# Kernel tuning notes

Measured on AMD Instinct MI355X. Metric: run time of the kernel, lower is better.

Reference implementation:

```python
import jax, jax.numpy as jnp
import numpy as np

N_EMBD = 2048
HEAD_SIZE = 64  # ln1.weight.shape[0] // n_head = 2048 // 32


def setup_inputs() -> dict:
    key = jax.random.key(0)
    ks = jax.random.split(key, 10)
    B, S, D = 4, 2048, N_EMBD
    return {
        'x': jax.random.normal(ks[0], (B, S, D), jnp.float32),
        'state': jax.random.normal(ks[1], (B, 2 + HEAD_SIZE, D), jnp.float32),
        'time_maa_x': jax.random.uniform(ks[2], (D,), jnp.float32),
        'time_maa_w1': jax.random.normal(ks[3], (D, 160), jnp.float32) * 0.02,
        'time_maa_w2': jax.random.normal(ks[4], (5, 32, D), jnp.float32) * 0.02,
        'maa_k': jax.random.uniform(ks[5], (D,), jnp.float32),
        'maa_w': jax.random.uniform(ks[6], (D,), jnp.float32),
        'maa_v': jax.random.uniform(ks[7], (D,), jnp.float32),
        'maa_r': jax.random.uniform(ks[8], (D,), jnp.float32),
        'maa_g': jax.random.uniform(ks[9], (D,), jnp.float32),
        'i': 0,
    }


def reference(x, state, time_maa_x, time_maa_w1, time_maa_w2,
              maa_k, maa_w, maa_v, maa_r, maa_g, i):
    B, S, D = x.shape
    i1 = (2 + HEAD_SIZE) * i + 1  # state row holding last token of this layer
    # token shift: sx[t] = x[t-1] - x[t], with state row for t=0
    sx = jnp.concatenate([(state[:, i1] - x[:, 0])[:, None],
                          x[:, :-1] - x[:, 1:]], axis=1)  # [B,S,D]
    new_state = state.at[:, i1].set(x[:, -1])
    # LoRA-style mixing coefficients
    xxx = jnp.tanh((x + sx * time_maa_x) @ time_maa_w1)       # [B,S,160]
    xxx = xxx.reshape(B, S, 5, 32)
    xxx = jnp.einsum('bsfk,fkd->bsfd', xxx, time_maa_w2)      # [B,S,5,D]
    stacked = jnp.stack([maa_k, maa_w, maa_v, maa_r, maa_g], axis=0)  # [5,D]
    # broadcast combine across the 5 mixing modes (k,w,v,r,g)
    x_kwvrg = x[:, :, None] + sx[:, :, None] * (stacked + xxx)  # [B,S,5,D]
    return x_kwvrg, new_state
```

## Files before the change

kernel.cpp:

```cpp
#include <hip/hip_runtime.h>

#define DDIM 2048
#define SLEN 2048
#define BSZ 4
#define NTOK (BSZ*SLEN)
#define RANK 160
#define SROWS 66
#define OUT_MAIN ((size_t)NTOK*5*DDIM)
#define STATE_N (BSZ*SROWS*DDIM)

typedef __bf16 bf16x8 __attribute__((ext_vector_type(8)));
typedef float  f32x4  __attribute__((ext_vector_type(4)));
typedef unsigned short us8 __attribute__((ext_vector_type(8)));

__device__ __forceinline__ unsigned short f2bf(float f) {
    unsigned b = __float_as_uint(f);
    return (unsigned short)((b + 0x7fffu + ((b >> 16) & 1u)) >> 16);
}

__global__ void k_state(const float* __restrict__ x,
                        const float* __restrict__ state,
                        const int* __restrict__ pi,
                        float* __restrict__ out_state) {
    int t = blockIdx.x * blockDim.x + threadIdx.x;
    int idx = t * 4;
    if (idx >= STATE_N) return;
    int i1 = 66 * pi[0] + 1;
    int b   = idx / (SROWS * DDIM);
    int rem = idx - b * (SROWS * DDIM);
    int row = rem / DDIM;
    int d   = rem - row * DDIM;
    f32x4 v;
    if (row == i1) v = *(const f32x4*)(x + ((size_t)(b * SLEN + SLEN - 1)) * DDIM + d);
    else           v = *(const f32x4*)(state + idx);
    *(f32x4*)(out_state + idx) = v;
}

__global__ void k_t_w1(const float* __restrict__ w1,
                       unsigned short* __restrict__ w1t) {
    int o = blockIdx.x * blockDim.x + threadIdx.x;
    if (o >= RANK * DDIM) return;
    int n = o >> 11;
    int k = o & (DDIM - 1);
    w1t[o] = f2bf(w1[k * RANK + n]);
}

__global__ void k_t_w2(const float* __restrict__ w2,
                       unsigned short* __restrict__ w2t) {
    int o = blockIdx.x * blockDim.x + threadIdx.x;
    if (o >= 5 * DDIM * 32) return;
    int k  = o & 31;
    int fd = o >> 5;
    int d  = fd & (DDIM - 1);
    int f  = fd >> 11;
    w2t[o] = f2bf(w2[(f * 32 + k) * DDIM + d]);
}

__global__ __launch_bounds__(256) void k_gemm1f(
        const float* __restrict__ x,
        const float* __restrict__ state,
        const float* __restrict__ tmx,
        const unsigned short* __restrict__ w1t,
        const int* __restrict__ pi,
        unsigned short* __restrict__ xxx) {
    __shared__ unsigned short sxw[32 * 88];
    int tid  = threadIdx.x;
    int w    = tid >> 6, lane = tid & 63;
    int q    = lane >> 4, nl = lane & 15;
    int msub = w & 1, nh = w >> 1;
    int m0   = blockIdx.x * 32;
    int b    = m0 >> 11;
    int i1   = 66 * pi[0] + 1;

    int srow = tid >> 3;
    int scol = (tid & 7) * 8;
    int m    = m0 + srow;
    int s    = m & (SLEN - 1);
    const float* xrow = x + (size_t)m * DDIM;
    const float* prow = (s == 0)
        ? (state + (size_t)(b * SROWS + i1) * DDIM)
        : (x + (size_t)(m - 1) * DDIM);

    f32x4 acc[5];
    #pragma unroll
    for (int t = 0; t < 5; t++) acc[t] = (f32x4){0.f, 0.f, 0.f, 0.f};

    for (int k0 = 0; k0 < DDIM; k0 += 64) {
        f32x4 xa = *(const f32x4*)(xrow + k0 + scol);
        f32x4 xb = *(const f32x4*)(xrow + k0 + scol + 4);
        f32x4 pa = *(const f32x4*)(prow + k0 + scol);
        f32x4 pb = *(const f32x4*)(prow + k0 + scol + 4);
        f32x4 ta = *(const f32x4*)(tmx  + k0 + scol);
        f32x4 tb = *(const f32x4*)(tmx  + k0 + scol + 4);
        us8 o;
        #pragma unroll
        for (int j = 0; j < 4; j++) {
            o[j]     = f2bf(xa[j] + (pa[j] - xa[j]) * ta[j]);
            o[j + 4] = f2bf(xb[j] + (pb[j] - xb[j]) * tb[j]);
        }
        *(us8*)(sxw + srow * 88 + scol) = o;
        __syncthreads();

        #pragma unroll
        for (int kk = 0; kk < 64; kk += 32) {
            bf16x8 a = *(const bf16x8*)(sxw + (msub * 16 + nl) * 88 + kk + q * 8);
            #pragma unroll
            for (int t = 0; t < 5; t++) {
                bf16x8 bb = *(const bf16x8*)(w1t + (size_t)(nh * 80 + t * 16 + nl) * DDIM
                                             + k0 + kk + q * 8);
                acc[t] = __builtin_amdgcn_mfma_f32_16x16x32_bf16(a, bb, acc[t], 0, 0, 0);
            }
        }
        __syncthreads();
    }

    #pragma unroll
    for (int t = 0; t < 5; t++)
        #pragma unroll
        for (int r = 0; r < 4; r++) {
            int mm = m0 + msub * 16 + q * 4 + r;
            int nn = nh * 80 + t * 16 + nl;
            xxx[mm * RANK + nn] = f2bf(tanhf(acc[t][r]));
        }
}

__global__ __launch_bounds__(256) void k_gemm2_out(
        const unsigned short* __restrict__ xxx,
        const unsigned short* __restrict__ w2t,
        const float* __restrict__ x,
        const float* __restrict__ state,
        const float* __restrict__ mk,
        const float* __restrict__ mw,
        const float* __restrict__ mv,
        const float* __restrict__ mr,
        const float* __restrict__ mg,
        const int* __restrict__ pi,
        float* __restrict__ out) {
    __shared__ float res[5 * 16 * 132];
    int tid = threadIdx.x;
    int w = tid >> 6, lane = tid & 63;
    int q = lane >> 4, nl = lane & 15;
    int tokTile = blockIdx.x >> 4;
    int dTile   = blockIdx.x & 15;
    int m0 = tokTile * 16;
    int d0 = dTile * 128;

    for (int t = w; t < 40; t += 4) {
        int f = t >> 3, dsub = t & 7;
        bf16x8 a = *(const bf16x8*)(xxx + (size_t)(m0 + nl) * RANK + f * 32 + q * 8);
        bf16x8 b = *(const bf16x8*)(w2t + ((size_t)(f * DDIM) + d0 + dsub * 16 + nl) * 32 + q * 8);
        f32x4 acc = (f32x4){0.f, 0.f, 0.f, 0.f};
        acc = __builtin_amdgcn_mfma_f32_16x16x32_bf16(a, b, acc, 0, 0, 0);
        #pragma unroll
        for (int r = 0; r < 4; r++)
            res[(f * 16 + q * 4 + r) * 132 + dsub * 16 + nl] = acc[r];
    }
    __syncthreads();

    int i1 = 66 * pi[0] + 1;
    const float* maas[5] = {mk, mw, mv, mr, mg};
    int b     = m0 >> 11;
    int sbase = m0 & (SLEN - 1);
    #pragma unroll
    for (int it = 0; it < 10; it++) {
        int g   = it * 256 + tid;
        int tok = g / 160;
        int r2  = g - tok * 160;
        int f   = r2 >> 5;
        int dv  = (r2 & 31) * 4;
        int s   = sbase + tok;
        int d   = d0 + dv;
        size_t xoff = ((size_t)(b * SLEN + s)) * DDIM + d;
        f32x4 xv = *(const f32x4*)(x + xoff);
        f32x4 pv;
        if (s == 0) pv = *(const f32x4*)(state + ((size_t)(b * SROWS + i1)) * DDIM + d);
        else        pv = *(const f32x4*)(x + xoff - DDIM);
        f32x4 mvv = *(const f32x4*)(maas[f] + d);
        f32x4 rr  = *(const f32x4*)&res[(f * 16 + tok) * 132 + dv];
        f32x4 o;
        #pragma unroll
        for (int j = 0; j < 4; j++) {
            float xf = xv[j];
            float sx = pv[j] - xf;
            o[j] = xf + sx * (mvv[j] + rr[j]);
        }
        *(f32x4*)(out + ((size_t)((b * SLEN + s) * 5 + f)) * DDIM + d) = o;
    }
}

extern "C" void kernel_launch(void* const* d_in, const int* in_sizes, int n_in,
                              void* d_out, int out_size, void* d_ws, size_t ws_size,
                              hipStream_t stream) {
    const float* x   = (const float*)d_in[0];
    const float* st  = (const float*)d_in[1];
    const float* tmx = (const float*)d_in[2];
    const float* w1  = (const float*)d_in[3];
    const float* w2  = (const float*)d_in[4];
    const float* mk  = (const float*)d_in[5];
    const float* mw  = (const float*)d_in[6];
    const float* mv  = (const float*)d_in[7];
    const float* mr  = (const float*)d_in[8];
    const float* mg  = (const float*)d_in[9];
    const int* pi    = (const int*)d_in[10];
    float* out = (float*)d_out;

    char* ws = (char*)d_ws;
    unsigned short* xxx = (unsigned short*)(ws);
    unsigned short* w1t = (unsigned short*)(ws + 2621440);
    unsigned short* w2t = (unsigned short*)(ws + 2621440 + 655360);

    k_state<<<528, 256, 0, stream>>>(x, st, pi, out + OUT_MAIN);
    k_t_w1<<<1280, 256, 0, stream>>>(w1, w1t);
    k_t_w2<<<1280, 256, 0, stream>>>(w2, w2t);
    k_gemm1f<<<256, 256, 0, stream>>>(x, st, tmx, w1t, pi, xxx);
    k_gemm2_out<<<8192, 256, 0, stream>>>(xxx, w2t, x, st, mk, mw, mv, mr, mg, pi, out);
}
```

Baseline: 501.9 us.

## Merge prep kernels, split-K gemm1 across more blocks, reorganize output loop

Fuses the state copy and the two weight transposes into one launch, with the transposes now staged through shared memory so reads and writes are coalesced. The first GEMM moves to 16-token tiles in 640-thread blocks that split K in two halves, combined through shared memory, which doubles the block count and raises parallelism. The output kernel now loads x and the previous row once per token and reuses them for all five modes, instead of reloading them per mode. The cost is an extra shared-memory reduction, a larger block size, and less register-level reuse of the weights in the first GEMM.

```diff
diff --git a/kernel.cpp b/kernel.cpp
--- a/kernel.cpp
+++ b/kernel.cpp
@@ -12,116 +12,140 @@
 typedef __bf16 bf16x8 __attribute__((ext_vector_type(8)));
 typedef float  f32x4  __attribute__((ext_vector_type(4)));
 typedef unsigned short us8 __attribute__((ext_vector_type(8)));
+typedef unsigned short us4 __attribute__((ext_vector_type(4)));
 
 __device__ __forceinline__ unsigned short f2bf(float f) {
     unsigned b = __float_as_uint(f);
     return (unsigned short)((b + 0x7fffu + ((b >> 16) & 1u)) >> 16);
 }
 
-__global__ void k_state(const float* __restrict__ x,
-                        const float* __restrict__ state,
-                        const int* __restrict__ pi,
-                        float* __restrict__ out_state) {
-    int t = blockIdx.x * blockDim.x + threadIdx.x;
-    int idx = t * 4;
-    if (idx >= STATE_N) return;
-    int i1 = 66 * pi[0] + 1;
-    int b   = idx / (SROWS * DDIM);
-    int rem = idx - b * (SROWS * DDIM);
-    int row = rem / DDIM;
-    int d   = rem - row * DDIM;
-    f32x4 v;
-    if (row == i1) v = *(const f32x4*)(x + ((size_t)(b * SLEN + SLEN - 1)) * DDIM + d);
-    else           v = *(const f32x4*)(state + idx);
-    *(f32x4*)(out_state + idx) = v;
-}
-
-__global__ void k_t_w1(const float* __restrict__ w1,
-                       unsigned short* __restrict__ w1t) {
-    int o = blockIdx.x * blockDim.x + threadIdx.x;
-    if (o >= RANK * DDIM) return;
-    int n = o >> 11;
-    int k = o & (DDIM - 1);
-    w1t[o] = f2bf(w1[k * RANK + n]);
-}
-
-__global__ void k_t_w2(const float* __restrict__ w2,
-                       unsigned short* __restrict__ w2t) {
-    int o = blockIdx.x * blockDim.x + threadIdx.x;
-    if (o >= 5 * DDIM * 32) return;
-    int k  = o & 31;
-    int fd = o >> 5;
-    int d  = fd & (DDIM - 1);
-    int f  = fd >> 11;
-    w2t[o] = f2bf(w2[(f * 32 + k) * DDIM + d]);
-}
-
-__global__ __launch_bounds__(256) void k_gemm1f(
+__global__ __launch_bounds__(256) void k_prep(
+        const float* __restrict__ x,
+        const float* __restrict__ state,
+        const int* __restrict__ pi,
+        const float* __restrict__ w1,
+        const float* __restrict__ w2,
+        float* __restrict__ out_state,
+        unsigned short* __restrict__ w1t,
+        unsigned short* __restrict__ w2t) {
+    __shared__ float t[32 * 33];
+    int bid = blockIdx.x, tid = threadIdx.x;
+    if (bid < 320) {
+        int kt = bid / 5;
+        int k0 = kt * 32, n0 = (bid - kt * 5) * 32;
+        int rr = tid >> 3, cc = (tid & 7) * 4;
+        f32x4 v = *(const f32x4*)(w1 + (size_t)(k0 + rr) * RANK + n0 + cc);
+        #pragma unroll
+        for (int j = 0; j < 4; j++) t[(cc + j) * 33 + rr] = v[j];
+        __syncthreads();
+        us4 o;
+        #pragma unroll
+        for (int j = 0; j < 4; j++) o[j] = f2bf(t[rr * 33 + cc + j]);
+        *(us4*)(w1t + (size_t)(n0 + rr) * DDIM + k0 + cc) = o;
+    } else if (bid < 640) {
+        int b2 = bid - 320;
+        int f = b2 >> 6, d0 = (b2 & 63) * 32;
+        int rr = tid >> 3, cc = (tid & 7) * 4;
+        f32x4 v = *(const f32x4*)(w2 + (size_t)(f * 32 + rr) * DDIM + d0 + cc);
+        #pragma unroll
+        for (int j = 0; j < 4; j++) t[(cc + j) * 33 + rr] = v[j];
+        __syncthreads();
+        us4 o;
+        #pragma unroll
+        for (int j = 0; j < 4; j++) o[j] = f2bf(t[rr * 33 + cc + j]);
+        *(us4*)(w2t + ((size_t)(f * DDIM) + d0 + rr) * 32 + cc) = o;
+    } else {
+        int idx = ((bid - 640) * 256 + tid) * 4;
+        int i1 = 66 * pi[0] + 1;
+        int b   = idx / (SROWS * DDIM);
+        int rem = idx - b * (SROWS * DDIM);
+        int row = rem / DDIM;
+        int d   = rem - row * DDIM;
+        f32x4 v;
+        if (row == i1) v = *(const f32x4*)(x + ((size_t)(b * SLEN + SLEN - 1)) * DDIM + d);
+        else           v = *(const f32x4*)(state + idx);
+        *(f32x4*)(out_state + idx) = v;
+    }
+}
+
+__global__ __launch_bounds__(640) void k_gemm1f(
         const float* __restrict__ x,
         const float* __restrict__ state,
         const float* __restrict__ tmx,
         const unsigned short* __restrict__ w1t,
         const int* __restrict__ pi,
         unsigned short* __restrict__ xxx) {
-    __shared__ unsigned short sxw[32 * 88];
+    __shared__ unsigned short sxw[16 * 136];
+    __shared__ float red[10 * 16 * 17];
     int tid  = threadIdx.x;
     int w    = tid >> 6, lane = tid & 63;
     int q    = lane >> 4, nl = lane & 15;
-    int msub = w & 1, nh = w >> 1;
-    int m0   = blockIdx.x * 32;
+    int kh   = (w >= 5) ? 1 : 0;
+    int nh   = kh ? (w - 5) : w;
+    int m0   = blockIdx.x * 16;
     int b    = m0 >> 11;
     int i1   = 66 * pi[0] + 1;
 
-    int srow = tid >> 3;
-    int scol = (tid & 7) * 8;
-    int m    = m0 + srow;
-    int s    = m & (SLEN - 1);
-    const float* xrow = x + (size_t)m * DDIM;
-    const float* prow = (s == 0)
-        ? (state + (size_t)(b * SROWS + i1) * DDIM)
-        : (x + (size_t)(m - 1) * DDIM);
-
-    f32x4 acc[5];
-    #pragma unroll
-    for (int t = 0; t < 5; t++) acc[t] = (f32x4){0.f, 0.f, 0.f, 0.f};
-
-    for (int k0 = 0; k0 < DDIM; k0 += 64) {
-        f32x4 xa = *(const f32x4*)(xrow + k0 + scol);
-        f32x4 xb = *(const f32x4*)(xrow + k0 + scol + 4);
-        f32x4 pa = *(const f32x4*)(prow + k0 + scol);
-        f32x4 pb = *(const f32x4*)(prow + k0 + scol + 4);
-        f32x4 ta = *(const f32x4*)(tmx  + k0 + scol);
-        f32x4 tb = *(const f32x4*)(tmx  + k0 + scol + 4);
-        us8 o;
-        #pragma unroll
-        for (int j = 0; j < 4; j++) {
-            o[j]     = f2bf(xa[j] + (pa[j] - xa[j]) * ta[j]);
-            o[j + 4] = f2bf(xb[j] + (pb[j] - xb[j]) * tb[j]);
+    int srow = tid >> 5;
+    int scol = (tid & 31) * 4;
+    const float* xrow = nullptr;
+    const float* prow = nullptr;
+    if (tid < 512) {
+        int m = m0 + srow;
+        int s = m & (SLEN - 1);
+        xrow = x + (size_t)m * DDIM;
+        prow = (s == 0) ? (state + (size_t)(b * SROWS + i1) * DDIM)
+                        : (x + (size_t)(m - 1) * DDIM);
+    }
+
+    f32x4 acc[2];
+    acc[0] = (f32x4){0.f, 0.f, 0.f, 0.f};
+    acc[1] = (f32x4){0.f, 0.f, 0.f, 0.f};
+
+    for (int i = 0; i < 16; i++) {
+        if (tid < 512) {
+            int gc = i * 128 + scol;
+            f32x4 xa = *(const f32x4*)(xrow + gc);
+            f32x4 pa = *(const f32x4*)(prow + gc);
+            f32x4 ta = *(const f32x4*)(tmx  + gc);
+            us4 o;
+            #pragma unroll
+            for (int j = 0; j < 4; j++)
+                o[j] = f2bf(xa[j] + (pa[j] - xa[j]) * ta[j]);
+            *(us4*)(sxw + srow * 136 + scol) = o;
         }
-        *(us8*)(sxw + srow * 88 + scol) = o;
-        __syncthreads();
-
+        __syncthreads();
         #pragma unroll
         for (int kk = 0; kk < 64; kk += 32) {
-            bf16x8 a = *(const bf16x8*)(sxw + (msub * 16 + nl) * 88 + kk + q * 8);
-            #pragma unroll
-            for (int t = 0; t < 5; t++) {
-                bf16x8 bb = *(const bf16x8*)(w1t + (size_t)(nh * 80 + t * 16 + nl) * DDIM
-                                             + k0 + kk + q * 8);
+            bf16x8 a = *(const bf16x8*)(sxw + nl * 136 + kh * 64 + kk + q * 8);
+            #pragma unroll
+            for (int t = 0; t < 2; t++) {
+                bf16x8 bb = *(const bf16x8*)(w1t + (size_t)(nh * 32 + t * 16 + nl) * DDIM
+                                             + i * 128 + kh * 64 + kk + q * 8);
                 acc[t] = __builtin_amdgcn_mfma_f32_16x16x32_bf16(a, bb, acc[t], 0, 0, 0);
             }
         }
         __syncthreads();
     }
 
-    #pragma unroll
-    for (int t = 0; t < 5; t++)
-        #pragma unroll
-        for (int r = 0; r < 4; r++) {
-            int mm = m0 + msub * 16 + q * 4 + r;
-            int nn = nh * 80 + t * 16 + nl;
-            xxx[mm * RANK + nn] = f2bf(tanhf(acc[t][r]));
-        }
+    if (kh) {
+        #pragma unroll
+        for (int t = 0; t < 2; t++)
+            #pragma unroll
+            for (int r = 0; r < 4; r++)
+                red[((nh * 2 + t) * 16 + q * 4 + r) * 17 + nl] = acc[t][r];
+    }
+    __syncthreads();
+    if (!kh) {
+        #pragma unroll
+        for (int t = 0; t < 2; t++)
+            #pragma unroll
+            for (int r = 0; r < 4; r++) {
+                float v = acc[t][r] + red[((nh * 2 + t) * 16 + q * 4 + r) * 17 + nl];
+                xxx[(size_t)(m0 + q * 4 + r) * RANK + nh * 32 + t * 16 + nl]
+                    = f2bf(tanhf(v));
+            }
+    }
 }
 
 __global__ __launch_bounds__(256) void k_gemm2_out(
@@ -158,16 +182,13 @@
     __syncthreads();
 
     int i1 = 66 * pi[0] + 1;
-    const float* maas[5] = {mk, mw, mv, mr, mg};
     int b     = m0 >> 11;
     int sbase = m0 & (SLEN - 1);
     #pragma unroll
-    for (int it = 0; it < 10; it++) {
-        int g   = it * 256 + tid;
-        int tok = g / 160;
-        int r2  = g - tok * 160;
-        int f   = r2 >> 5;
-        int dv  = (r2 & 31) * 4;
+    for (int half = 0; half < 2; half++) {
+        int tt  = half * 256 + tid;
+        int tok = tt >> 5;
+        int dv  = (tt & 31) * 4;
         int s   = sbase + tok;
         int d   = d0 + dv;
         size_t xoff = ((size_t)(b * SLEN + s)) * DDIM + d;
@@ -175,16 +196,22 @@
         f32x4 pv;
         if (s == 0) pv = *(const f32x4*)(state + ((size_t)(b * SROWS + i1)) * DDIM + d);
         else        pv = *(const f32x4*)(x + xoff - DDIM);
-        f32x4 mvv = *(const f32x4*)(maas[f] + d);
-        f32x4 rr  = *(const f32x4*)&res[(f * 16 + tok) * 132 + dv];
-        f32x4 o;
-        #pragma unroll
-        for (int j = 0; j < 4; j++) {
-            float xf = xv[j];
-            float sx = pv[j] - xf;
-            o[j] = xf + sx * (mvv[j] + rr[j]);
+        size_t obase = ((size_t)((b * SLEN + s) * 5)) * DDIM + d;
+        #pragma unroll
+        for (int f = 0; f < 5; f++) {
+            const float* maa = (f == 0) ? mk : (f == 1) ? mw : (f == 2) ? mv
+                             : (f == 3) ? mr : mg;
+            f32x4 mvv = *(const f32x4*)(maa + d);
+            f32x4 rr  = *(const f32x4*)&res[(f * 16 + tok) * 132 + dv];
+            f32x4 o;
+            #pragma unroll
+            for (int j = 0; j < 4; j++) {
+                float xf = xv[j];
+                float sx = pv[j] - xf;
+                o[j] = xf + sx * (mvv[j] + rr[j]);
+            }
+            *(f32x4*)(out + obase + (size_t)f * DDIM) = o;
         }
-        *(f32x4*)(out + ((size_t)((b * SLEN + s) * 5 + f)) * DDIM + d) = o;
     }
 }
 
@@ -209,9 +236,7 @@
     unsigned short* w1t = (unsigned short*)(ws + 2621440);
     unsigned short* w2t = (unsigned short*)(ws + 2621440 + 655360);
 
-    k_state<<<528, 256, 0, stream>>>(x, st, pi, out + OUT_MAIN);
-    k_t_w1<<<1280, 256, 0, stream>>>(w1, w1t);
-    k_t_w2<<<1280, 256, 0, stream>>>(w2, w2t);
-    k_gemm1f<<<256, 256, 0, stream>>>(x, st, tmx, w1t, pi, xxx);
+    k_prep<<<1168, 256, 0, stream>>>(x, st, pi, w1, w2, out + OUT_MAIN, w1t, w2t);
+    k_gemm1f<<<512, 640, 0, stream>>>(x, st, tmx, w1t, pi, xxx);
     k_gemm2_out<<<8192, 256, 0, stream>>>(xxx, w2t, x, st, mk, mw, mv, mr, mg, pi, out);
 }
```

Result: faster. 459.6 us (-8.4%).
